# Performance work log

Measured on AMD Instinct MI355X. Metric: run time of the kernel, lower is better.

The kernel has to match this reference:

```python
import jax, jax.numpy as jnp
import numpy as np

TRIANGLE_TABLE = np.array([
    [-1,-1,-1,-1,-1,-1],[1,0,2,-1,-1,-1],[4,0,3,-1,-1,-1],[1,4,2,1,3,4],
    [3,1,5,-1,-1,-1],[2,3,0,2,5,3],[1,4,0,1,5,4],[4,2,5,-1,-1,-1],
    [4,5,2,-1,-1,-1],[4,1,0,4,5,1],[3,2,0,3,5,2],[1,3,5,-1,-1,-1],
    [4,1,2,4,3,1],[3,0,4,-1,-1,-1],[2,0,1,-1,-1,-1],[-1,-1,-1,-1,-1,-1]], dtype=np.int64)
NUM_TRIANGLES_TABLE = np.array([0,1,1,2,1,2,2,1,1,2,2,1,2,1,1,0], dtype=np.int64)
BASE_TET_EDGES = np.array([0,1,0,2,0,3,1,2,1,3,2,3], dtype=np.int64)


def _topology(sdf_np, tet_np):
    """Integer/no-grad part of marching tets (matches torch.no_grad block)."""
    occ = sdf_np > 0                                   # [N]
    occ_f4 = occ[tet_np]                               # [F,4]
    occ_sum = occ_f4.sum(-1)
    valid = (occ_sum > 0) & (occ_sum < 4)              # surface-crossing tets
    tets = tet_np[valid]                               # [T,4]
    edges = tets[:, BASE_TET_EDGES].reshape(-1, 2)     # [T*6,2]
    edges = np.sort(edges, axis=1)                     # canonical (min,max) == sort_edges
    unique_edges, idx_map = np.unique(edges, axis=0, return_inverse=True)
    idx_map = idx_map.reshape(-1)
    mask_edges = occ[unique_edges].sum(-1) == 1        # edges crossing the surface
    mapping = np.full(unique_edges.shape[0], -1, dtype=np.int64)
    mapping[mask_edges] = np.arange(int(mask_edges.sum()), dtype=np.int64)
    idx_map = mapping[idx_map].reshape(-1, 6)          # per-tet edge->vert ids
    interp_v = unique_edges[mask_edges]                # [M,2] endpoints to interpolate
    v_id = 1 << np.arange(4, dtype=np.int64)
    tetindex = (occ_f4[valid].astype(np.int64) * v_id).sum(-1)   # [T] case index 0..15
    num_tri = NUM_TRIANGLES_TABLE[tetindex]
    tt = TRIANGLE_TABLE[tetindex]
    faces1 = np.take_along_axis(idx_map[num_tri == 1], tt[num_tri == 1][:, :3], axis=1).reshape(-1, 3)
    faces2 = np.take_along_axis(idx_map[num_tri == 2], tt[num_tri == 2][:, :6], axis=1).reshape(-1, 3)
    faces = np.concatenate([faces1, faces2], axis=0)
    return interp_v, faces


def setup_inputs() -> dict:
    key = jax.random.key(0)
    k1, k2, k3 = jax.random.split(key, 3)
    N, F = 300000, 1500000
    pos_nx3 = jax.random.normal(k1, (N, 3), dtype=jnp.float32)
    sdf_n = jax.random.normal(k2, (N,), dtype=jnp.float32)
    tet_fx4 = jax.random.randint(k3, (F, 4), 0, N, dtype=jnp.int64)
    return {"pos_nx3": pos_nx3, "sdf_n": sdf_n, "tet_fx4": tet_fx4}


def reference(pos_nx3, sdf_n, tet_fx4):
    # topology (index-valued, non-differentiable) computed on host
    interp_v, faces = _topology(np.asarray(sdf_n), np.asarray(tet_fx4))
    iv = jnp.asarray(interp_v)                         # [M,2]
    ep = pos_nx3[iv]                                   # [M,2,3] endpoint positions
    es = sdf_n[iv] * jnp.array([1.0, -1.0], dtype=sdf_n.dtype)  # [M,2] = (a, -b)
    denom = es.sum(axis=1, keepdims=True)              # a - b
    w = es[:, ::-1] / denom                            # flip: (-b, a)/(a-b)
    verts = (ep * w[..., None]).sum(axis=1)            # linear interpolation at sdf=0
    return verts, jnp.asarray(faces)
```

## Files before the change

### kernel.cpp

```cpp
#include <hip/hip_runtime.h>
#include <stdint.h>

static __device__ __constant__ int d_TRI[16][6] = {
  {-1,-1,-1,-1,-1,-1},{1,0,2,-1,-1,-1},{4,0,3,-1,-1,-1},{1,4,2,1,3,4},
  {3,1,5,-1,-1,-1},{2,3,0,2,5,3},{1,4,0,1,5,4},{4,2,5,-1,-1,-1},
  {4,5,2,-1,-1,-1},{4,1,0,4,5,1},{3,2,0,3,5,2},{1,3,5,-1,-1,-1},
  {4,1,2,4,3,1},{3,0,4,-1,-1,-1},{2,0,1,-1,-1,-1},{-1,-1,-1,-1,-1,-1}};
static __device__ __constant__ int d_NT[16] = {0,1,1,2,1,2,2,1,1,2,2,1,2,1,1,0};
static __device__ __constant__ int d_EA[6] = {0,0,0,1,1,2};
static __device__ __constant__ int d_EB[6] = {1,2,3,2,3,3};

__device__ __forceinline__ void wave_sync_lds() {
  __builtin_amdgcn_sched_barrier(0);
  asm volatile("s_waitcnt lgkmcnt(0)" ::: "memory");
  __builtin_amdgcn_sched_barrier(0);
}
__device__ __forceinline__ void wave_sync_vm() {
  __builtin_amdgcn_sched_barrier(0);
  asm volatile("s_waitcnt vmcnt(0)" ::: "memory");
  __builtin_amdgcn_sched_barrier(0);
}

#define SB 256
#define SI 8
#define STILE (SB*SI)

__global__ void k_scan_partial(const unsigned* __restrict__ in, unsigned* __restrict__ bsum, int n) {
  int b = blockIdx.x;
  int base = b * STILE;
  __shared__ unsigned sh[SB];
  unsigned s = 0;
  for (int i = threadIdx.x; i < STILE; i += SB) {
    int idx = base + i;
    s += (idx < n) ? in[idx] : 0u;
  }
  sh[threadIdx.x] = s; __syncthreads();
  for (int st = SB/2; st > 0; st >>= 1) {
    if (threadIdx.x < st) sh[threadIdx.x] += sh[threadIdx.x + st];
    __syncthreads();
  }
  if (threadIdx.x == 0) bsum[b] = sh[0];
}

__global__ void k_scan_mid(const unsigned* __restrict__ bsum, unsigned* __restrict__ boff,
                           int B, unsigned* __restrict__ total_dst) {
  int t = threadIdx.x;
  unsigned loc[SI];
  int base = t * SI;
  unsigned s = 0;
  #pragma unroll
  for (int i = 0; i < SI; ++i) {
    int idx = base + i;
    unsigned v = (idx < B) ? bsum[idx] : 0u;
    loc[i] = s; s += v;
  }
  __shared__ unsigned sh[SB];
  sh[t] = s; __syncthreads();
  for (int o = 1; o < SB; o <<= 1) {
    unsigned v = (t >= o) ? sh[t - o] : 0u;
    __syncthreads();
    sh[t] += v;
    __syncthreads();
  }
  unsigned texcl = sh[t] - s;
  #pragma unroll
  for (int i = 0; i < SI; ++i) {
    int idx = base + i;
    if (idx < B) boff[idx] = texcl + loc[i];
  }
  if (t == SB - 1 && total_dst) *total_dst = sh[SB - 1];
}

__global__ void k_scan_final(const unsigned* __restrict__ in, const unsigned* __restrict__ boff,
                             unsigned* __restrict__ out, int n) {
  int b = blockIdx.x;
  int base = b * STILE + threadIdx.x * SI;
  unsigned loc[SI];
  unsigned s = 0;
  #pragma unroll
  for (int i = 0; i < SI; ++i) {
    int idx = base + i;
    unsigned v = (idx < n) ? in[idx] : 0u;
    loc[i] = s; s += v;
  }
  __shared__ unsigned sh[SB];
  int t = threadIdx.x;
  sh[t] = s; __syncthreads();
  for (int o = 1; o < SB; o <<= 1) {
    unsigned v = (t >= o) ? sh[t - o] : 0u;
    __syncthreads();
    sh[t] += v;
    __syncthreads();
  }
  unsigned texcl = sh[t] - s;
  unsigned bo = boff[b];
  #pragma unroll
  for (int i = 0; i < SI; ++i) {
    int idx = base + i;
    if (idx < n) out[idx] = bo + texcl + loc[i];
  }
}


__global__ void k_classify(const int* __restrict__ tet, const float* __restrict__ sdf,
                           unsigned* __restrict__ cnt, unsigned* __restrict__ t12, int F) {
  int f = blockIdx.x * blockDim.x + threadIdx.x;
  if (f >= F) return;
  int4 q = reinterpret_cast<const int4*>(tet)[f];
  int v[4] = {q.x, q.y, q.z, q.w};
  int oc[4];
  #pragma unroll
  for (int i = 0; i < 4; ++i) oc[i] = sdf[v[i]] > 0.0f;
  int s = oc[0] + oc[1] + oc[2] + oc[3];
  int valid = (s > 0) & (s < 4);
  int tix = oc[0] | (oc[1] << 1) | (oc[2] << 2) | (oc[3] << 3);
  int nt = valid ? d_NT[tix] : 0;
  t12[f] = (nt == 1) ? 1u : 0u;
  t12[F + f] = (nt == 2) ? 1u : 0u;
  if (!valid) return;
  #pragma unroll
  for (int e = 0; e < 6; ++e) {
    int a = v[d_EA[e]], b = v[d_EB[e]];
    if (oc[d_EA[e]] != oc[d_EB[e]]) {
      int lo = a < b ? a : b;
      atomicAdd(&cnt[lo], 1u);
    }
  }
}

__global__ void k_scatter(const int* __restrict__ tet, const float* __restrict__ sdf,
                          unsigned* __restrict__ off, unsigned* __restrict__ inst, int F) {
  int f = blockIdx.x * blockDim.x + threadIdx.x;
  if (f >= F) return;
  int4 q = reinterpret_cast<const int4*>(tet)[f];
  int v[4] = {q.x, q.y, q.z, q.w};
  int oc[4];
  #pragma unroll
  for (int i = 0; i < 4; ++i) oc[i] = sdf[v[i]] > 0.0f;
  int s = oc[0] + oc[1] + oc[2] + oc[3];
  if (s == 0 || s == 4) return;
  #pragma unroll
  for (int e = 0; e < 6; ++e) {
    int a = v[d_EA[e]], b = v[d_EB[e]];
    if (oc[d_EA[e]] != oc[d_EB[e]]) {
      int lo = a < b ? a : b;
      int hi = a < b ? b : a;
      unsigned p = atomicAdd(&off[lo], 1u);
      inst[p] = (unsigned)hi;
    }
  }
}

#define CAP 512
__global__ void k_sortdedupe(const unsigned* __restrict__ off, const unsigned* __restrict__ cnt,
                             unsigned* __restrict__ inst, unsigned* __restrict__ gtmp,
                             unsigned* __restrict__ ucnt, int N) {
  __shared__ unsigned sA[4][CAP];
  __shared__ unsigned sBv[4][CAP];
  int w = threadIdx.x >> 6;
  int lane = threadIdx.x & 63;
  int v0 = blockIdx.x * 4 + w;
  if (v0 >= N) return;
  unsigned n = cnt[v0];
  if (n == 0) { if (lane == 0) ucnt[v0] = 0u; return; }
  unsigned base = off[v0] - n;

  if (n <= CAP) {
    for (unsigned k = lane; k < n; k += 64) sA[w][k] = inst[base + k];
    wave_sync_lds();
    for (unsigned k = lane; k < n; k += 64) {
      unsigned val = sA[w][k];
      unsigned r = 0;
      for (unsigned j = 0; j < n; ++j) {
        unsigned x = sA[w][j];
        r += (x < val) || (x == val && j < k);
      }
      sBv[w][r] = val;
    }
    wave_sync_lds();
    unsigned ub = 0;
    for (unsigned c = 0; c < n; c += 64) {
      unsigned k = c + (unsigned)lane;
      bool act = k < n;
      unsigned val = act ? sBv[w][k] : 0u;
      bool flag = act && (k == 0 || val != sBv[w][k - 1]);
      unsigned long long m = __ballot((int)flag);
      if (flag) {
        unsigned pos = ub + (unsigned)__popcll(m & ((1ull << lane) - 1ull));
        inst[base + pos] = val;
      }
      ub += (unsigned)__popcll(m);
    }
    if (lane == 0) ucnt[v0] = ub;
  } else {
    for (unsigned k = lane; k < n; k += 64) {
      unsigned val = inst[base + k];
      unsigned r = 0;
      for (unsigned j = 0; j < n; ++j) {
        unsigned x = inst[base + j];
        r += (x < val) || (x == val && j < k);
      }
      gtmp[base + r] = val;
    }
    wave_sync_vm();
    __threadfence_block();
    if (lane == 0) {
      unsigned u = 0, prev = 0xFFFFFFFFu;
      for (unsigned k = 0; k < n; ++k) {
        unsigned val = gtmp[base + k];
        if (k == 0 || val != prev) { inst[base + u++] = val; prev = val; }
      }
      ucnt[v0] = u;
    }
  }
}

__global__ void k_verts(const unsigned* __restrict__ off, const unsigned* __restrict__ cnt,
                        const unsigned* __restrict__ uoff, const unsigned* __restrict__ ucnt,
                        const unsigned* __restrict__ inst, unsigned* __restrict__ uniq,
                        const float* __restrict__ pos, const float* __restrict__ sdf,
                        float* __restrict__ out, int N) {
  int w = threadIdx.x >> 6;
  int lane = threadIdx.x & 63;
  int v0 = blockIdx.x * 4 + w;
  if (v0 >= N) return;
  unsigned u = ucnt[v0];
  if (u == 0) return;
  unsigned base = off[v0] - cnt[v0];
  unsigned ub = uoff[v0];
  float a = sdf[v0];
  float p0x = pos[3 * (size_t)v0 + 0], p0y = pos[3 * (size_t)v0 + 1], p0z = pos[3 * (size_t)v0 + 2];
  for (unsigned k = lane; k < u; k += 64) {
    unsigned v1 = inst[base + k];
    unsigned r = ub + k;
    uniq[r] = v1;
    float b = sdf[v1];
    float d = a - b;
    float w0 = -b / d;
    float w1 = a / d;
    size_t ro = (size_t)3 * r;
    out[ro + 0] = p0x * w0 + pos[3 * (size_t)v1 + 0] * w1;
    out[ro + 1] = p0y * w0 + pos[3 * (size_t)v1 + 1] * w1;
    out[ro + 2] = p0z * w0 + pos[3 * (size_t)v1 + 2] * w1;
  }
}

__global__ void k_faces(const int* __restrict__ tet, const float* __restrict__ sdf,
                        const unsigned* __restrict__ uoff, const unsigned* __restrict__ ucnt,
                        const unsigned* __restrict__ uniq, const unsigned* __restrict__ C,
                        float* __restrict__ out, int F, int N) {
  int f = blockIdx.x * blockDim.x + threadIdx.x;
  if (f >= F) return;
  int4 q = reinterpret_cast<const int4*>(tet)[f];
  int v[4] = {q.x, q.y, q.z, q.w};
  int oc[4];
  #pragma unroll
  for (int i = 0; i < 4; ++i) oc[i] = sdf[v[i]] > 0.0f;
  int s = oc[0] + oc[1] + oc[2] + oc[3];
  if (s == 0 || s == 4) return;
  int tix = oc[0] | (oc[1] << 1) | (oc[2] << 2) | (oc[3] << 3);
  int nt = d_NT[tix];
  int rank[6];
  #pragma unroll
  for (int e = 0; e < 6; ++e) {
    int a = v[d_EA[e]], b = v[d_EB[e]];
    if (oc[d_EA[e]] != oc[d_EB[e]]) {
      int lo = a < b ? a : b;
      int hi = a < b ? b : a;
      unsigned lbase = uoff[lo];
      unsigned len = ucnt[lo];
      unsigned loI = 0, hiI = len;
      while (loI < hiI) {
        unsigned mid = (loI + hiI) >> 1;
        if ((int)uniq[lbase + mid] < hi) loI = mid + 1; else hiI = mid;
      }
      rank[e] = (int)(lbase + loI);
    } else {
      rank[e] = -1;
    }
  }
  unsigned M = uoff[N];
  float* fo = out + (size_t)3 * M;
  const int* tt = d_TRI[tix];
  if (nt == 1) {
    unsigned r = C[f];
    size_t o = (size_t)3 * r;
    fo[o + 0] = (float)rank[tt[0]];
    fo[o + 1] = (float)rank[tt[1]];
    fo[o + 2] = (float)rank[tt[2]];
  } else {
    unsigned T1 = C[F];
    unsigned r0 = T1 + 2u * (C[F + f] - T1);
    size_t o = (size_t)3 * r0;
    #pragma unroll
    for (int c = 0; c < 6; ++c) fo[o + c] = (float)rank[tt[c]];
  }
}

static void run_scan(const unsigned* in, unsigned* out, int n,
                     unsigned* bsum, unsigned* boff, hipStream_t s) {
  int B = (n + STILE - 1) / STILE;
  k_scan_partial<<<B, SB, 0, s>>>(in, bsum, n);
  k_scan_mid<<<1, SB, 0, s>>>(bsum, boff, B, out + n);
  k_scan_final<<<B, SB, 0, s>>>(in, boff, out, n);
}

extern "C" void kernel_launch(void* const* d_in, const int* in_sizes, int n_in,
                              void* d_out, int out_size, void* d_ws, size_t ws_size,
                              hipStream_t stream) {
  const float* pos = (const float*)d_in[0];
  const float* sdf = (const float*)d_in[1];
  const int* tet = (const int*)d_in[2];
  int N = in_sizes[1];
  int F = in_sizes[2] / 4;
  float* out = (float*)d_out;

  char* w = (char*)d_ws;
  size_t o = 0;
  auto take = [&](size_t bytes) -> char* {
    char* p = w + o;
    o = (o + bytes + 255) & ~(size_t)255;
    return p;
  };
  unsigned* cnt  = (unsigned*)take((size_t)(N + 1) * 4);
  unsigned* off  = (unsigned*)take((size_t)(N + 1) * 4);
  unsigned* ucnt = (unsigned*)take((size_t)(N + 1) * 4);
  unsigned* uoff = (unsigned*)take((size_t)(N + 1) * 4);
  unsigned* t12  = (unsigned*)take((size_t)2 * F * 4);
  unsigned* C    = (unsigned*)take(((size_t)2 * F + 1) * 4);
  unsigned* inst = (unsigned*)take((size_t)4 * F * 4);
  unsigned* uniq = (unsigned*)take((size_t)4 * F * 4);
  unsigned* bsum = (unsigned*)take(4096 * 4);
  unsigned* boff = (unsigned*)take(4096 * 4);

  int TB = 256;
  int FB = (F + TB - 1) / TB;
  int NB4 = (N + 3) / 4;

  hipMemsetAsync(cnt, 0, (size_t)N * 4, stream);
  k_classify<<<FB, TB, 0, stream>>>(tet, sdf, cnt, t12, F);
  run_scan(cnt, off, N, bsum, boff, stream);
  k_scatter<<<FB, TB, 0, stream>>>(tet, sdf, off, inst, F);
  k_sortdedupe<<<NB4, TB, 0, stream>>>(off, cnt, inst, uniq, ucnt, N);
  run_scan(ucnt, uoff, N, bsum, boff, stream);
  k_verts<<<NB4, TB, 0, stream>>>(off, cnt, uoff, ucnt, inst, uniq, pos, sdf, out, N);
  run_scan(t12, C, 2 * F, bsum, boff, stream);
  k_faces<<<FB, TB, 0, stream>>>(tet, sdf, uoff, ucnt, uniq, C, out, F, N);
}
```

Measured before the change: 970.7 us.

## Bucket edges by 8-vertex groups, cache occupancy bytes, and block-level face scans

Edge instances are now grouped into buckets of 8 lower vertices, with counters spread across 8 slots per bucket by block index to reduce atomic contention. Each bucket is sorted and deduplicated by one wave, and the local rank of each unique edge is packed into the stored word. Per-tet occupancy codes are written once as bytes so scatter and faces no longer re-gather sdf. The face-count scan shrinks from per-tet to per-block totals plus an in-block scan, and the binary search in faces becomes a linear probe. The costs are larger sort groups per wave, a serial fallback for oversized buckets, and packed fields that assume vertex ids below 2^19.

```diff
diff --git a/kernel.cpp b/kernel.cpp
--- a/kernel.cpp
+++ b/kernel.cpp
@@ -1,5 +1,7 @@
 #include <hip/hip_runtime.h>
 #include <stdint.h>
+
+#define TB 256
 
 static __device__ __constant__ int d_TRI[16][6] = {
   {-1,-1,-1,-1,-1,-1},{1,0,2,-1,-1,-1},{4,0,3,-1,-1,-1},{1,4,2,1,3,4},
@@ -15,11 +17,6 @@
   asm volatile("s_waitcnt lgkmcnt(0)" ::: "memory");
   __builtin_amdgcn_sched_barrier(0);
 }
-__device__ __forceinline__ void wave_sync_vm() {
-  __builtin_amdgcn_sched_barrier(0);
-  asm volatile("s_waitcnt vmcnt(0)" ::: "memory");
-  __builtin_amdgcn_sched_barrier(0);
-}
 
 #define SB 256
 #define SI 8
@@ -101,70 +98,94 @@
   }
 }
 
+__global__ void k_copy_u32(unsigned* __restrict__ dst, const unsigned* __restrict__ src, int n) {
+  int i = blockIdx.x * blockDim.x + threadIdx.x;
+  if (i < n) dst[i] = src[i];
+}
 
 __global__ void k_classify(const int* __restrict__ tet, const float* __restrict__ sdf,
-                           unsigned* __restrict__ cnt, unsigned* __restrict__ t12, int F) {
-  int f = blockIdx.x * blockDim.x + threadIdx.x;
+                           unsigned* __restrict__ cnt8, unsigned char* __restrict__ occb,
+                           unsigned* __restrict__ bs, int F, int FB) {
+  int f = blockIdx.x * TB + threadIdx.x;
+  unsigned pk = 0;
+  int xg = blockIdx.x & 7;
+  if (f < F) {
+    int4 q = reinterpret_cast<const int4*>(tet)[f];
+    int v[4] = {q.x, q.y, q.z, q.w};
+    int oc[4];
+    #pragma unroll
+    for (int i = 0; i < 4; ++i) oc[i] = sdf[v[i]] > 0.0f;
+    int tix = oc[0] | (oc[1] << 1) | (oc[2] << 2) | (oc[3] << 3);
+    occb[f] = (unsigned char)tix;
+    int nt = d_NT[tix];
+    pk = (nt == 1 ? 1u : 0u) | (nt == 2 ? 0x10000u : 0u);
+    if (nt > 0) {
+      #pragma unroll
+      for (int e = 0; e < 6; ++e) {
+        int ai = d_EA[e], bi = d_EB[e];
+        if (oc[ai] != oc[bi]) {
+          int a = v[ai], b = v[bi];
+          int lo = a < b ? a : b;
+          atomicAdd(&cnt8[(lo & ~7) + xg], 1u);
+        }
+      }
+    }
+  }
+  __shared__ unsigned sh[TB];
+  sh[threadIdx.x] = pk; __syncthreads();
+  for (int st = TB/2; st > 0; st >>= 1) {
+    if (threadIdx.x < st) sh[threadIdx.x] += sh[threadIdx.x + st];
+    __syncthreads();
+  }
+  if (threadIdx.x == 0) {
+    unsigned t = sh[0];
+    bs[blockIdx.x] = t & 0xFFFFu;
+    bs[FB + blockIdx.x] = t >> 16;
+  }
+}
+
+__global__ void k_scatter(const int* __restrict__ tet, const unsigned char* __restrict__ occb,
+                          unsigned* __restrict__ cur8, unsigned* __restrict__ inst, int F) {
+  int f = blockIdx.x * TB + threadIdx.x;
   if (f >= F) return;
+  int tix = occb[f];
+  if (tix == 0 || tix == 15) return;
   int4 q = reinterpret_cast<const int4*>(tet)[f];
   int v[4] = {q.x, q.y, q.z, q.w};
-  int oc[4];
-  #pragma unroll
-  for (int i = 0; i < 4; ++i) oc[i] = sdf[v[i]] > 0.0f;
-  int s = oc[0] + oc[1] + oc[2] + oc[3];
-  int valid = (s > 0) & (s < 4);
-  int tix = oc[0] | (oc[1] << 1) | (oc[2] << 2) | (oc[3] << 3);
-  int nt = valid ? d_NT[tix] : 0;
-  t12[f] = (nt == 1) ? 1u : 0u;
-  t12[F + f] = (nt == 2) ? 1u : 0u;
-  if (!valid) return;
+  int xg = blockIdx.x & 7;
   #pragma unroll
   for (int e = 0; e < 6; ++e) {
-    int a = v[d_EA[e]], b = v[d_EB[e]];
-    if (oc[d_EA[e]] != oc[d_EB[e]]) {
-      int lo = a < b ? a : b;
-      atomicAdd(&cnt[lo], 1u);
-    }
-  }
-}
-
-__global__ void k_scatter(const int* __restrict__ tet, const float* __restrict__ sdf,
-                          unsigned* __restrict__ off, unsigned* __restrict__ inst, int F) {
-  int f = blockIdx.x * blockDim.x + threadIdx.x;
-  if (f >= F) return;
-  int4 q = reinterpret_cast<const int4*>(tet)[f];
-  int v[4] = {q.x, q.y, q.z, q.w};
-  int oc[4];
-  #pragma unroll
-  for (int i = 0; i < 4; ++i) oc[i] = sdf[v[i]] > 0.0f;
-  int s = oc[0] + oc[1] + oc[2] + oc[3];
-  if (s == 0 || s == 4) return;
-  #pragma unroll
-  for (int e = 0; e < 6; ++e) {
-    int a = v[d_EA[e]], b = v[d_EB[e]];
-    if (oc[d_EA[e]] != oc[d_EB[e]]) {
+    int ai = d_EA[e], bi = d_EB[e];
+    int oa = (tix >> ai) & 1, ob = (tix >> bi) & 1;
+    if (oa != ob) {
+      int a = v[ai], b = v[bi];
       int lo = a < b ? a : b;
       int hi = a < b ? b : a;
-      unsigned p = atomicAdd(&off[lo], 1u);
-      inst[p] = (unsigned)hi;
+      unsigned p = atomicAdd(&cur8[(lo & ~7) + xg], 1u);
+      inst[p] = ((unsigned)(lo & 7) << 19) | (unsigned)hi;
     }
   }
 }
 
 #define CAP 512
-__global__ void k_sortdedupe(const unsigned* __restrict__ off, const unsigned* __restrict__ cnt,
-                             unsigned* __restrict__ inst, unsigned* __restrict__ gtmp,
-                             unsigned* __restrict__ ucnt, int N) {
+__global__ void k_sortdedupe(const unsigned* __restrict__ off8, unsigned* __restrict__ inst,
+                             unsigned* __restrict__ gtmp, unsigned* __restrict__ ucnt,
+                             unsigned* __restrict__ ucB, int CB, int N) {
   __shared__ unsigned sA[4][CAP];
-  __shared__ unsigned sBv[4][CAP];
+  __shared__ unsigned sD[4][CAP];
   int w = threadIdx.x >> 6;
   int lane = threadIdx.x & 63;
-  int v0 = blockIdx.x * 4 + w;
-  if (v0 >= N) return;
-  unsigned n = cnt[v0];
-  if (n == 0) { if (lane == 0) ucnt[v0] = 0u; return; }
-  unsigned base = off[v0] - n;
-
+  int cb = blockIdx.x * 4 + w;
+  if (cb >= CB) return;
+  int k8 = cb * 8;
+  int k8e = k8 + 8; if (k8e > N) k8e = N;
+  unsigned base = off8[k8];
+  unsigned n = off8[k8e] - base;
+  if (n == 0) {
+    if (lane < 8 && k8 + lane < N) ucnt[k8 + lane] = 0u;
+    if (lane == 0) ucB[cb] = 0u;
+    return;
+  }
   if (n <= CAP) {
     for (unsigned k = lane; k < n; k += 64) sA[w][k] = inst[base + k];
     wave_sync_lds();
@@ -175,122 +196,141 @@
         unsigned x = sA[w][j];
         r += (x < val) || (x == val && j < k);
       }
-      sBv[w][r] = val;
+      sD[w][r] = val;
     }
     wave_sync_lds();
     unsigned ub = 0;
     for (unsigned c = 0; c < n; c += 64) {
       unsigned k = c + (unsigned)lane;
       bool act = k < n;
-      unsigned val = act ? sBv[w][k] : 0u;
-      bool flag = act && (k == 0 || val != sBv[w][k - 1]);
+      unsigned val = act ? sD[w][k] : 0u;
+      bool flag = act && (k == 0 || val != sD[w][k - 1]);
       unsigned long long m = __ballot((int)flag);
       if (flag) {
         unsigned pos = ub + (unsigned)__popcll(m & ((1ull << lane) - 1ull));
-        inst[base + pos] = val;
+        sA[w][pos] = val;
       }
       ub += (unsigned)__popcll(m);
     }
-    if (lane == 0) ucnt[v0] = ub;
+    wave_sync_lds();
+    for (unsigned k = lane; k < ub; k += 64) {
+      unsigned e = sA[w][k];
+      unsigned l19 = e >> 19;
+      unsigned j = k;
+      while (j > 0 && (sA[w][j - 1] >> 19) == l19) --j;
+      inst[base + k] = ((k - j) << 22) | (e & 0x3FFFFFu);
+    }
+    if (lane < 8 && k8 + lane < N) {
+      unsigned c = 0;
+      for (unsigned j = 0; j < ub; ++j) c += ((sA[w][j] >> 19) == (unsigned)lane);
+      ucnt[k8 + lane] = c;
+    }
+    if (lane == 0) ucB[cb] = ub;
   } else {
-    for (unsigned k = lane; k < n; k += 64) {
-      unsigned val = inst[base + k];
-      unsigned r = 0;
-      for (unsigned j = 0; j < n; ++j) {
-        unsigned x = inst[base + j];
-        r += (x < val) || (x == val && j < k);
+    if (lane == 0) {
+      unsigned u = 0, prev = 0; bool first = true;
+      unsigned uc[8] = {0,0,0,0,0,0,0,0};
+      while (true) {
+        unsigned m = 0xFFFFFFFFu;
+        for (unsigned j = 0; j < n; ++j) {
+          unsigned x = inst[base + j] & 0x3FFFFFu;
+          if ((first || x > prev) && x < m) m = x;
+        }
+        if (m == 0xFFFFFFFFu) break;
+        unsigned l = m >> 19;
+        gtmp[base + u] = (uc[l] << 22) | m;
+        uc[l]++; u++; prev = m; first = false;
       }
-      gtmp[base + r] = val;
-    }
-    wave_sync_vm();
-    __threadfence_block();
-    if (lane == 0) {
-      unsigned u = 0, prev = 0xFFFFFFFFu;
-      for (unsigned k = 0; k < n; ++k) {
-        unsigned val = gtmp[base + k];
-        if (k == 0 || val != prev) { inst[base + u++] = val; prev = val; }
-      }
-      ucnt[v0] = u;
-    }
-  }
-}
-
-__global__ void k_verts(const unsigned* __restrict__ off, const unsigned* __restrict__ cnt,
-                        const unsigned* __restrict__ uoff, const unsigned* __restrict__ ucnt,
-                        const unsigned* __restrict__ inst, unsigned* __restrict__ uniq,
-                        const float* __restrict__ pos, const float* __restrict__ sdf,
-                        float* __restrict__ out, int N) {
+      for (unsigned j = 0; j < u; ++j) inst[base + j] = gtmp[base + j];
+      for (int l = 0; l < 8; ++l) if (k8 + l < N) ucnt[k8 + l] = uc[l];
+      ucB[cb] = u;
+    }
+  }
+}
+
+__global__ void k_verts(const unsigned* __restrict__ off8, const unsigned* __restrict__ ucB,
+                        const unsigned* __restrict__ uoff, const unsigned* __restrict__ inst,
+                        unsigned* __restrict__ uniq, const float* __restrict__ pos,
+                        const float* __restrict__ sdf, float* __restrict__ out, int CB) {
   int w = threadIdx.x >> 6;
   int lane = threadIdx.x & 63;
-  int v0 = blockIdx.x * 4 + w;
-  if (v0 >= N) return;
-  unsigned u = ucnt[v0];
+  int cb = blockIdx.x * 4 + w;
+  if (cb >= CB) return;
+  unsigned u = ucB[cb];
   if (u == 0) return;
-  unsigned base = off[v0] - cnt[v0];
-  unsigned ub = uoff[v0];
-  float a = sdf[v0];
-  float p0x = pos[3 * (size_t)v0 + 0], p0y = pos[3 * (size_t)v0 + 1], p0z = pos[3 * (size_t)v0 + 2];
+  unsigned base = off8[cb * 8];
   for (unsigned k = lane; k < u; k += 64) {
-    unsigned v1 = inst[base + k];
-    unsigned r = ub + k;
-    uniq[r] = v1;
-    float b = sdf[v1];
+    unsigned e = inst[base + k];
+    unsigned hi = e & 0x7FFFFu;
+    unsigned l3 = (e >> 19) & 7u;
+    unsigned idx = e >> 22;
+    unsigned lo = (unsigned)cb * 8u + l3;
+    unsigned r = uoff[lo] + idx;
+    uniq[r] = hi;
+    float a = sdf[lo];
+    float b = sdf[hi];
     float d = a - b;
     float w0 = -b / d;
     float w1 = a / d;
     size_t ro = (size_t)3 * r;
-    out[ro + 0] = p0x * w0 + pos[3 * (size_t)v1 + 0] * w1;
-    out[ro + 1] = p0y * w0 + pos[3 * (size_t)v1 + 1] * w1;
-    out[ro + 2] = p0z * w0 + pos[3 * (size_t)v1 + 2] * w1;
-  }
-}
-
-__global__ void k_faces(const int* __restrict__ tet, const float* __restrict__ sdf,
-                        const unsigned* __restrict__ uoff, const unsigned* __restrict__ ucnt,
-                        const unsigned* __restrict__ uniq, const unsigned* __restrict__ C,
-                        float* __restrict__ out, int F, int N) {
-  int f = blockIdx.x * blockDim.x + threadIdx.x;
-  if (f >= F) return;
+    out[ro + 0] = pos[3 * (size_t)lo + 0] * w0 + pos[3 * (size_t)hi + 0] * w1;
+    out[ro + 1] = pos[3 * (size_t)lo + 1] * w0 + pos[3 * (size_t)hi + 1] * w1;
+    out[ro + 2] = pos[3 * (size_t)lo + 2] * w0 + pos[3 * (size_t)hi + 2] * w1;
+  }
+}
+
+__global__ void k_faces(const int* __restrict__ tet, const unsigned char* __restrict__ occb,
+                        const unsigned* __restrict__ uoff, const unsigned* __restrict__ uniq,
+                        const unsigned* __restrict__ C, float* __restrict__ out,
+                        int F, int FB, int N) {
+  int f = blockIdx.x * TB + threadIdx.x;
+  int tix = (f < F) ? (int)occb[f] : 0;
+  int nt = d_NT[tix];
+  unsigned pk = (nt == 1 ? 1u : 0u) | (nt == 2 ? 0x10000u : 0u);
+  __shared__ unsigned sh[TB];
+  int t = threadIdx.x;
+  sh[t] = pk; __syncthreads();
+  for (int o = 1; o < TB; o <<= 1) {
+    unsigned v = (t >= o) ? sh[t - o] : 0u;
+    __syncthreads();
+    sh[t] += v;
+    __syncthreads();
+  }
+  unsigned excl = sh[t] - pk;
+  if (f >= F || nt == 0) return;
+  unsigned C1b = C[blockIdx.x];
+  unsigned T1 = C[FB];
+  unsigned C2b = C[FB + blockIdx.x] - T1;
+  unsigned M = uoff[N];
   int4 q = reinterpret_cast<const int4*>(tet)[f];
   int v[4] = {q.x, q.y, q.z, q.w};
-  int oc[4];
-  #pragma unroll
-  for (int i = 0; i < 4; ++i) oc[i] = sdf[v[i]] > 0.0f;
-  int s = oc[0] + oc[1] + oc[2] + oc[3];
-  if (s == 0 || s == 4) return;
-  int tix = oc[0] | (oc[1] << 1) | (oc[2] << 2) | (oc[3] << 3);
-  int nt = d_NT[tix];
   int rank[6];
   #pragma unroll
   for (int e = 0; e < 6; ++e) {
-    int a = v[d_EA[e]], b = v[d_EB[e]];
-    if (oc[d_EA[e]] != oc[d_EB[e]]) {
+    int ai = d_EA[e], bi = d_EB[e];
+    int oa = (tix >> ai) & 1, ob = (tix >> bi) & 1;
+    if (oa != ob) {
+      int a = v[ai], b = v[bi];
       int lo = a < b ? a : b;
       int hi = a < b ? b : a;
-      unsigned lbase = uoff[lo];
-      unsigned len = ucnt[lo];
-      unsigned loI = 0, hiI = len;
-      while (loI < hiI) {
-        unsigned mid = (loI + hiI) >> 1;
-        if ((int)uniq[lbase + mid] < hi) loI = mid + 1; else hiI = mid;
-      }
-      rank[e] = (int)(lbase + loI);
+      unsigned ubase = uoff[lo];
+      unsigned j = 0;
+      while (uniq[ubase + j] != (unsigned)hi) ++j;
+      rank[e] = (int)(ubase + j);
     } else {
       rank[e] = -1;
     }
   }
-  unsigned M = uoff[N];
   float* fo = out + (size_t)3 * M;
   const int* tt = d_TRI[tix];
   if (nt == 1) {
-    unsigned r = C[f];
+    unsigned r = C1b + (excl & 0xFFFFu);
     size_t o = (size_t)3 * r;
     fo[o + 0] = (float)rank[tt[0]];
     fo[o + 1] = (float)rank[tt[1]];
     fo[o + 2] = (float)rank[tt[2]];
   } else {
-    unsigned T1 = C[F];
-    unsigned r0 = T1 + 2u * (C[F + f] - T1);
+    unsigned r0 = T1 + 2u * (C2b + (excl >> 16));
     size_t o = (size_t)3 * r0;
     #pragma unroll
     for (int c = 0; c < 6; ++c) fo[o + c] = (float)rank[tt[c]];
@@ -322,28 +362,32 @@
     o = (o + bytes + 255) & ~(size_t)255;
     return p;
   };
-  unsigned* cnt  = (unsigned*)take((size_t)(N + 1) * 4);
-  unsigned* off  = (unsigned*)take((size_t)(N + 1) * 4);
+  int FB = (F + TB - 1) / TB;
+  int CB = (N + 7) / 8;
+  unsigned* cnt8 = (unsigned*)take((size_t)(N + 8) * 4);
+  unsigned* off8 = (unsigned*)take((size_t)(N + 8) * 4);
+  unsigned* cur8 = (unsigned*)take((size_t)(N + 8) * 4);
   unsigned* ucnt = (unsigned*)take((size_t)(N + 1) * 4);
   unsigned* uoff = (unsigned*)take((size_t)(N + 1) * 4);
-  unsigned* t12  = (unsigned*)take((size_t)2 * F * 4);
-  unsigned* C    = (unsigned*)take(((size_t)2 * F + 1) * 4);
+  unsigned* ucB  = (unsigned*)take((size_t)(CB + 1) * 4);
+  unsigned* bs   = (unsigned*)take((size_t)2 * FB * 4);
+  unsigned* C    = (unsigned*)take(((size_t)2 * FB + 1) * 4);
+  unsigned char* occb = (unsigned char*)take((size_t)F);
   unsigned* inst = (unsigned*)take((size_t)4 * F * 4);
   unsigned* uniq = (unsigned*)take((size_t)4 * F * 4);
   unsigned* bsum = (unsigned*)take(4096 * 4);
   unsigned* boff = (unsigned*)take(4096 * 4);
 
-  int TB = 256;
-  int FB = (F + TB - 1) / TB;
-  int NB4 = (N + 3) / 4;
-
-  hipMemsetAsync(cnt, 0, (size_t)N * 4, stream);
-  k_classify<<<FB, TB, 0, stream>>>(tet, sdf, cnt, t12, F);
-  run_scan(cnt, off, N, bsum, boff, stream);
-  k_scatter<<<FB, TB, 0, stream>>>(tet, sdf, off, inst, F);
-  k_sortdedupe<<<NB4, TB, 0, stream>>>(off, cnt, inst, uniq, ucnt, N);
+  int NBc = (CB + 3) / 4;
+
+  hipMemsetAsync(cnt8, 0, (size_t)N * 4, stream);
+  k_classify<<<FB, TB, 0, stream>>>(tet, sdf, cnt8, occb, bs, F, FB);
+  run_scan(cnt8, off8, N, bsum, boff, stream);
+  k_copy_u32<<<(N + TB - 1) / TB, TB, 0, stream>>>(cur8, off8, N);
+  k_scatter<<<FB, TB, 0, stream>>>(tet, occb, cur8, inst, F);
+  k_sortdedupe<<<NBc, TB, 0, stream>>>(off8, inst, uniq, ucnt, ucB, CB, N);
   run_scan(ucnt, uoff, N, bsum, boff, stream);
-  k_verts<<<NB4, TB, 0, stream>>>(off, cnt, uoff, ucnt, inst, uniq, pos, sdf, out, N);
-  run_scan(t12, C, 2 * F, bsum, boff, stream);
-  k_faces<<<FB, TB, 0, stream>>>(tet, sdf, uoff, ucnt, uniq, C, out, F, N);
-}
+  k_verts<<<NBc, TB, 0, stream>>>(off8, ucB, uoff, inst, uniq, pos, sdf, out, CB);
+  run_scan(bs, C, 2 * FB, bsum, boff, stream);
+  k_faces<<<FB, TB, 0, stream>>>(tet, occb, uoff, uniq, C, out, F, FB, N);
+}
```

Result: slower. 1.150 ms (+18.5%).
